# Kernel optimization log

Measured on AMD Instinct MI355X. Metric: run time of the kernel, lower is better.

## Reference

```python
import jax, jax.numpy as jnp
import numpy as np

D = 256
H = 4
HD = D // H


def setup_inputs() -> dict:
    key = jax.random.key(0)
    ks = jax.random.split(key, 12)
    A, T = 64, 512
    s = 1.0 / np.sqrt(D)
    return {
        "features": jax.random.normal(ks[0], (A, T, D), jnp.float32),
        "positions": jax.random.normal(ks[1], (A, T, 2), jnp.float32),
        "Wq": jax.random.normal(ks[2], (D, D), jnp.float32) * s,
        "bq": jnp.zeros((D,), jnp.float32),
        "Wk": jax.random.normal(ks[3], (D, D), jnp.float32) * s,
        "bk": jnp.zeros((D,), jnp.float32),
        "Wv": jax.random.normal(ks[4], (D, D), jnp.float32) * s,
        "bv": jnp.zeros((D,), jnp.float32),
        "Wo": jax.random.normal(ks[5], (D, D), jnp.float32) * s,
        "bo": jnp.zeros((D,), jnp.float32),
        "max_distance": 2,
        "time_window": 64,
    }


def _sparse_mask(positions, max_distance, time_window):
    # positions: [A, T, 2] -> allowed [A, T, T]
    A, T, _ = positions.shape
    diff = positions[:, :, None, :] - positions[:, None, :, :]  # [A,T,T,2]
    dist2 = jnp.sum(diff * diff, axis=-1)                       # [A,T,T]
    t = jnp.arange(T)
    tmask = jnp.abs(t[:, None] - t[None, :]) <= time_window      # [T,T]
    return (dist2 <= float(max_distance) ** 2) & tmask[None]     # [A,T,T]


def reference(features, positions, Wq, bq, Wk, bk, Wv, bv, Wo, bo,
              max_distance, time_window):
    A, T, Dm = features.shape
    allowed = _sparse_mask(positions, max_distance, time_window)  # [A,T,T]
    q = features @ Wq.T + bq
    k = features @ Wk.T + bk
    v = features @ Wv.T + bv
    # split heads: [A, T, H, HD]
    q = q.reshape(A, T, H, HD)
    k = k.reshape(A, T, H, HD)
    v = v.reshape(A, T, H, HD)
    scale = 1.0 / np.sqrt(HD)
    scores = jnp.einsum("athd,ashd->ahts", q, k) * scale          # [A,H,T,T]
    scores = jnp.where(allowed[:, None], scores, -jnp.inf)
    attn = jax.nn.softmax(scores, axis=-1)
    out = jnp.einsum("ahts,ashd->athd", attn, v).reshape(A, T, Dm)
    return out @ Wo.T + bo
```

## Files before the change

### kernel.cpp

```cpp
#include <hip/hip_runtime.h>
#include <hip/hip_bf16.h>
#include <cstdint>
#include <cstddef>

typedef __attribute__((ext_vector_type(8))) _Float16 half8;
typedef __attribute__((ext_vector_type(4))) _Float16 half4v;
typedef __attribute__((ext_vector_type(4))) float floatx4;

#define MFMA16(a, b, c) __builtin_amdgcn_mfma_f32_16x16x32_f16((a), (b), (c), 0, 0, 0)

#define NFEAT 8388608
#define NW    65536

__global__ __launch_bounds__(256) void convert_kernel(
    const float* __restrict__ feat, const float* __restrict__ wq,
    const float* __restrict__ wk, const float* __restrict__ wv,
    const float* __restrict__ wo, _Float16* __restrict__ out)
{
    long tid  = (long)blockIdx.x * blockDim.x + threadIdx.x;
    long base = tid * 4;
    if (base >= (long)NFEAT + 4L * NW) return;
    const float* src;
    long off;
    if (base < NFEAT) { src = feat; off = base; }
    else {
        long r = base - NFEAT;
        int  w = (int)(r >> 16);
        off = r & (NW - 1);
        src = (w == 0) ? wq : (w == 1) ? wk : (w == 2) ? wv : wo;
    }
    float4 v = *(const float4*)(src + off);
    half4v h = { (_Float16)v.x, (_Float16)v.y, (_Float16)v.z, (_Float16)v.w };
    *(half4v*)(out + base) = h;
}

template <bool OUT_HALF>
__device__ __forceinline__ void gemm_core(
    const _Float16* __restrict__ X, const _Float16* __restrict__ W,
    const float* __restrict__ bias, void* __restrict__ Cptr)
{
    __shared__ _Float16 Xs[128 * 40];
    __shared__ _Float16 Wsm[64 * 40];

    const int tid  = threadIdx.x;
    const int lane = tid & 63, wid = tid >> 6;
    const int quad = lane >> 4, l16 = lane & 15;
    const int wm = wid & 1, wn = wid >> 1;
    const int bm = blockIdx.x, bn = blockIdx.y;

    floatx4 acc[4][2] = {};

    const _Float16* Xg = X + (size_t)bm * 128 * 256;
    const _Float16* Wg = W + (size_t)bn * 64 * 256;

    for (int k0 = 0; k0 < 256; k0 += 32) {
#pragma unroll
        for (int i = 0; i < 2; ++i) {
            int c = tid + 256 * i;
            int row = c >> 2, col = (c & 3) * 8;
            *(half8*)(&Xs[row * 40 + col]) =
                *(const half8*)(Xg + (size_t)row * 256 + k0 + col);
        }
        {
            int row = tid >> 2, col = (tid & 3) * 8;
            *(half8*)(&Wsm[row * 40 + col]) =
                *(const half8*)(Wg + (size_t)row * 256 + k0 + col);
        }
        __syncthreads();

        half8 af[4], bf[2];
#pragma unroll
        for (int mi = 0; mi < 4; ++mi)
            af[mi] = *(const half8*)(&Xs[(wm * 64 + mi * 16 + l16) * 40 + quad * 8]);
#pragma unroll
        for (int ni = 0; ni < 2; ++ni)
            bf[ni] = *(const half8*)(&Wsm[(wn * 32 + ni * 16 + l16) * 40 + quad * 8]);
#pragma unroll
        for (int mi = 0; mi < 4; ++mi)
#pragma unroll
            for (int ni = 0; ni < 2; ++ni)
                acc[mi][ni] = MFMA16(af[mi], bf[ni], acc[mi][ni]);
        __syncthreads();
    }

#pragma unroll
    for (int ni = 0; ni < 2; ++ni) {
        int col = bn * 64 + wn * 32 + ni * 16 + l16;
        float bv = bias[col];
#pragma unroll
        for (int mi = 0; mi < 4; ++mi) {
#pragma unroll
            for (int r = 0; r < 4; ++r) {
                int row = bm * 128 + wm * 64 + mi * 16 + quad * 4 + r;
                float v = acc[mi][ni][r] + bv;
                if (OUT_HALF)
                    ((_Float16*)Cptr)[(size_t)row * 256 + col] = (_Float16)v;
                else
                    ((float*)Cptr)[(size_t)row * 256 + col] = v;
            }
        }
    }
}

__global__ __launch_bounds__(256) void qkv_gemm(
    const _Float16* __restrict__ featH, const _Float16* __restrict__ WH,
    const float* __restrict__ bq, const float* __restrict__ bk,
    const float* __restrict__ bv,
    _Float16* __restrict__ Qb, _Float16* __restrict__ Kb, _Float16* __restrict__ Vb)
{
    int z = blockIdx.z;
    const _Float16* W = WH + (size_t)z * NW;
    const float* bias = (z == 0) ? bq : (z == 1) ? bk : bv;
    _Float16* out    = (z == 0) ? Qb : (z == 1) ? Kb : Vb;
    gemm_core<true>(featH, W, bias, out);
}

__global__ __launch_bounds__(256) void out_gemm(
    const _Float16* __restrict__ attnH, const _Float16* __restrict__ WoH,
    const float* __restrict__ bo, float* __restrict__ out)
{
    gemm_core<false>(attnH, WoH, bo, out);
}

__global__ __launch_bounds__(256) void attn_kernel(
    const _Float16* __restrict__ Qb, const _Float16* __restrict__ Kb,
    const _Float16* __restrict__ Vb, const float* __restrict__ positions,
    const int* __restrict__ mdp, const int* __restrict__ twp,
    _Float16* __restrict__ attnb)
{
    const int qt = blockIdx.x, h = blockIdx.y, a = blockIdx.z;
    const int q0 = qt * 64;
    const int s_base = q0 - 64;
    const int tid = threadIdx.x, lane = tid & 63, wid = tid >> 6;
    const int quad = lane >> 4, l16 = lane & 15;

    __shared__ _Float16 KPs[192 * 72];
    __shared__ _Float16 Vt[64 * 200];
    __shared__ float qpos_s[128];
    __shared__ float kpos_s[384];

    const size_t abase = (size_t)a * 512;

#pragma unroll
    for (int i = 0; i < 6; ++i) {
        int c  = tid + 256 * i;
        int si = c >> 3, col = (c & 7) * 8;
        int sr = s_base + si;
        int sc = min(max(sr, 0), 511);
        *(half8*)(&KPs[si * 72 + col]) =
            *(const half8*)(Kb + (abase + sc) * 256 + h * 64 + col);
    }
#pragma unroll
    for (int i = 0; i < 6; ++i) {
        int c  = tid + 256 * i;
        int si = c >> 3, d0 = (c & 7) * 8;
        int sc = min(max(s_base + si, 0), 511);
        half8 v = *(const half8*)(Vb + (abase + sc) * 256 + h * 64 + d0);
#pragma unroll
        for (int j = 0; j < 8; ++j) Vt[(d0 + j) * 200 + si] = v[j];
    }
    if (tid < 128)
        qpos_s[tid] = positions[(abase + q0 + (tid >> 1)) * 2 + (tid & 1)];
    for (int i = tid; i < 384; i += 256) {
        int si = i >> 1;
        int sc = min(max(s_base + si, 0), 511);
        kpos_s[i] = positions[(abase + sc) * 2 + (i & 1)];
    }
    __syncthreads();

    const int md = *mdp, tw = *twp;
    const float md2 = (float)(md * md);

    const size_t qrow = abase + q0 + wid * 16 + l16;
    half8 aq0 = *(const half8*)(Qb + qrow * 256 + h * 64 + quad * 8);
    half8 aq1 = *(const half8*)(Qb + qrow * 256 + h * 64 + 32 + quad * 8);

    float qpx[4], qpy[4];
    int trow[4];
#pragma unroll
    for (int r = 0; r < 4; ++r) {
        int m = wid * 16 + quad * 4 + r;
        trow[r] = q0 + m;
        qpx[r] = qpos_s[m * 2];
        qpy[r] = qpos_s[m * 2 + 1];
    }

    floatx4 S[12];
#pragma unroll
    for (int j = 0; j < 12; ++j) {
        half8 bk0 = *(const half8*)(&KPs[(j * 16 + l16) * 72 + quad * 8]);
        half8 bk1 = *(const half8*)(&KPs[(j * 16 + l16) * 72 + 32 + quad * 8]);
        floatx4 acc = {};
        acc = MFMA16(aq0, bk0, acc);
        acc = MFMA16(aq1, bk1, acc);
        int si = j * 16 + l16;
        int sr = s_base + si;
        float kx = kpos_s[si * 2], ky = kpos_s[si * 2 + 1];
        bool svalid = (sr >= 0) && (sr < 512);
#pragma unroll
        for (int r = 0; r < 4; ++r) {
            float dx = qpx[r] - kx, dy = qpy[r] - ky;
            float d2 = dx * dx + dy * dy;
            int dt = trow[r] - sr; dt = dt < 0 ? -dt : dt;
            bool ok = svalid && (d2 <= md2) && (dt <= tw);
            S[j][r] = ok ? acc[r] * 0.125f : -1e30f;
        }
    }

    float minv[4];
#pragma unroll
    for (int r = 0; r < 4; ++r) {
        float m = -1e30f;
#pragma unroll
        for (int j = 0; j < 12; ++j) m = fmaxf(m, S[j][r]);
        m = fmaxf(m, __shfl_xor(m, 1));
        m = fmaxf(m, __shfl_xor(m, 2));
        m = fmaxf(m, __shfl_xor(m, 4));
        m = fmaxf(m, __shfl_xor(m, 8));
        float l = 0.f;
#pragma unroll
        for (int j = 0; j < 12; ++j) {
            float p = __expf(S[j][r] - m);
            S[j][r] = p;
            l += p;
        }
        l += __shfl_xor(l, 1);
        l += __shfl_xor(l, 2);
        l += __shfl_xor(l, 4);
        l += __shfl_xor(l, 8);
        minv[r] = 1.0f / l;
    }

    __syncthreads();

    _Float16* Ps = KPs + wid * 16 * 200;
#pragma unroll
    for (int j = 0; j < 12; ++j)
#pragma unroll
        for (int r = 0; r < 4; ++r)
            Ps[(quad * 4 + r) * 200 + j * 16 + l16] = (_Float16)(S[j][r] * minv[r]);

    half8 af[6];
#pragma unroll
    for (int k = 0; k < 6; ++k)
        af[k] = *(const half8*)(&Ps[l16 * 200 + k * 32 + quad * 8]);
#pragma unroll
    for (int n = 0; n < 4; ++n) {
        floatx4 accO = {};
#pragma unroll
        for (int k = 0; k < 6; ++k) {
            half8 bv = *(const half8*)(&Vt[(n * 16 + l16) * 200 + k * 32 + quad * 8]);
            accO = MFMA16(af[k], bv, accO);
        }
#pragma unroll
        for (int r = 0; r < 4; ++r) {
            int row = q0 + wid * 16 + quad * 4 + r;
            attnb[(abase + row) * 256 + h * 64 + n * 16 + l16] = (_Float16)accO[r];
        }
    }
}

extern "C" void kernel_launch(void* const* d_in, const int* in_sizes, int n_in,
                              void* d_out, int out_size, void* d_ws, size_t ws_size,
                              hipStream_t stream)
{
    const float* feat = (const float*)d_in[0];
    const float* pos  = (const float*)d_in[1];
    const float* Wq   = (const float*)d_in[2];
    const float* bq   = (const float*)d_in[3];
    const float* Wk   = (const float*)d_in[4];
    const float* bk   = (const float*)d_in[5];
    const float* Wv   = (const float*)d_in[6];
    const float* bv   = (const float*)d_in[7];
    const float* Wo   = (const float*)d_in[8];
    const float* bo   = (const float*)d_in[9];
    const int*   md   = (const int*)d_in[10];
    const int*   tw   = (const int*)d_in[11];
    float*       out  = (float*)d_out;

    _Float16* ws    = (_Float16*)d_ws;
    _Float16* featH = ws;
    _Float16* WH    = featH + NFEAT;
    _Float16* Qb    = WH + 4 * NW;
    _Float16* Kb    = Qb + NFEAT;
    _Float16* Vb    = Kb + NFEAT;
    _Float16* attnH = featH;

    convert_kernel<<<8448, 256, 0, stream>>>(feat, Wq, Wk, Wv, Wo, ws);

    dim3 gqkv(256, 4, 3);
    qkv_gemm<<<gqkv, 256, 0, stream>>>(featH, WH, bq, bk, bv, Qb, Kb, Vb);

    dim3 gattn(8, 4, 64);
    attn_kernel<<<gattn, 256, 0, stream>>>(Qb, Kb, Vb, pos, md, tw, attnH);

    dim3 gout(256, 4, 1);
    out_gemm<<<gout, 256, 0, stream>>>(attnH, WH + 3 * (size_t)NW, bo, out);
}
```

Baseline: 190.8 us.

## Widen GEMM tiles to full N, reorder grid, and streamline attention loads

The projection GEMMs now compute a 128x256 output tile per block (full N) instead of 128x64, so each feature tile is loaded once rather than four times. The grid order is changed so the Q/K/V blocks for the same row-block run adjacently. In attention, the V transpose-load mapping is reordered to improve LDS write patterns, and the position staging in shared memory is replaced by direct global float2 loads. The larger accumulator (32 floatx4 per thread) raises register pressure, and the out GEMM drops to 256 blocks, which may reduce occupancy.

```diff
diff --git a/kernel.cpp b/kernel.cpp
--- a/kernel.cpp
+++ b/kernel.cpp
@@ -35,23 +35,20 @@
 }
 
 template <bool OUT_HALF>
-__device__ __forceinline__ void gemm_core(
+__device__ __forceinline__ void gemm_core2(
     const _Float16* __restrict__ X, const _Float16* __restrict__ W,
-    const float* __restrict__ bias, void* __restrict__ Cptr)
+    const float* __restrict__ bias, void* __restrict__ Cptr, int bm)
 {
     __shared__ _Float16 Xs[128 * 40];
-    __shared__ _Float16 Wsm[64 * 40];
+    __shared__ _Float16 Ws[256 * 40];
 
     const int tid  = threadIdx.x;
     const int lane = tid & 63, wid = tid >> 6;
     const int quad = lane >> 4, l16 = lane & 15;
     const int wm = wid & 1, wn = wid >> 1;
-    const int bm = blockIdx.x, bn = blockIdx.y;
-
-    floatx4 acc[4][2] = {};
-
+
+    floatx4 acc[4][8] = {};
     const _Float16* Xg = X + (size_t)bm * 128 * 256;
-    const _Float16* Wg = W + (size_t)bn * 64 * 256;
 
     for (int k0 = 0; k0 < 256; k0 += 32) {
 #pragma unroll
@@ -61,31 +58,33 @@
             *(half8*)(&Xs[row * 40 + col]) =
                 *(const half8*)(Xg + (size_t)row * 256 + k0 + col);
         }
-        {
-            int row = tid >> 2, col = (tid & 3) * 8;
-            *(half8*)(&Wsm[row * 40 + col]) =
-                *(const half8*)(Wg + (size_t)row * 256 + k0 + col);
+#pragma unroll
+        for (int i = 0; i < 4; ++i) {
+            int c = tid + 256 * i;
+            int row = c >> 2, col = (c & 3) * 8;
+            *(half8*)(&Ws[row * 40 + col]) =
+                *(const half8*)(W + (size_t)row * 256 + k0 + col);
         }
         __syncthreads();
 
-        half8 af[4], bf[2];
+        half8 af[4], bf[8];
 #pragma unroll
         for (int mi = 0; mi < 4; ++mi)
             af[mi] = *(const half8*)(&Xs[(wm * 64 + mi * 16 + l16) * 40 + quad * 8]);
 #pragma unroll
-        for (int ni = 0; ni < 2; ++ni)
-            bf[ni] = *(const half8*)(&Wsm[(wn * 32 + ni * 16 + l16) * 40 + quad * 8]);
+        for (int ni = 0; ni < 8; ++ni)
+            bf[ni] = *(const half8*)(&Ws[(wn * 128 + ni * 16 + l16) * 40 + quad * 8]);
 #pragma unroll
         for (int mi = 0; mi < 4; ++mi)
 #pragma unroll
-            for (int ni = 0; ni < 2; ++ni)
+            for (int ni = 0; ni < 8; ++ni)
                 acc[mi][ni] = MFMA16(af[mi], bf[ni], acc[mi][ni]);
         __syncthreads();
     }
 
 #pragma unroll
-    for (int ni = 0; ni < 2; ++ni) {
-        int col = bn * 64 + wn * 32 + ni * 16 + l16;
+    for (int ni = 0; ni < 8; ++ni) {
+        int col = wn * 128 + ni * 16 + l16;
         float bv = bias[col];
 #pragma unroll
         for (int mi = 0; mi < 4; ++mi) {
@@ -102,24 +101,24 @@
     }
 }
 
-__global__ __launch_bounds__(256) void qkv_gemm(
+__global__ __launch_bounds__(256, 2) void qkv_gemm(
     const _Float16* __restrict__ featH, const _Float16* __restrict__ WH,
     const float* __restrict__ bq, const float* __restrict__ bk,
     const float* __restrict__ bv,
     _Float16* __restrict__ Qb, _Float16* __restrict__ Kb, _Float16* __restrict__ Vb)
 {
-    int z = blockIdx.z;
+    int z = blockIdx.x;
     const _Float16* W = WH + (size_t)z * NW;
     const float* bias = (z == 0) ? bq : (z == 1) ? bk : bv;
     _Float16* out    = (z == 0) ? Qb : (z == 1) ? Kb : Vb;
-    gemm_core<true>(featH, W, bias, out);
-}
-
-__global__ __launch_bounds__(256) void out_gemm(
+    gemm_core2<true>(featH, W, bias, out, blockIdx.y);
+}
+
+__global__ __launch_bounds__(256, 2) void out_gemm(
     const _Float16* __restrict__ attnH, const _Float16* __restrict__ WoH,
     const float* __restrict__ bo, float* __restrict__ out)
 {
-    gemm_core<false>(attnH, WoH, bo, out);
+    gemm_core2<false>(attnH, WoH, bo, out, blockIdx.y);
 }
 
 __global__ __launch_bounds__(256) void attn_kernel(
@@ -136,8 +135,6 @@
 
     __shared__ _Float16 KPs[192 * 72];
     __shared__ _Float16 Vt[64 * 200];
-    __shared__ float qpos_s[128];
-    __shared__ float kpos_s[384];
 
     const size_t abase = (size_t)a * 512;
 
@@ -145,26 +142,19 @@
     for (int i = 0; i < 6; ++i) {
         int c  = tid + 256 * i;
         int si = c >> 3, col = (c & 7) * 8;
-        int sr = s_base + si;
-        int sc = min(max(sr, 0), 511);
+        int sc = min(max(s_base + si, 0), 511);
         *(half8*)(&KPs[si * 72 + col]) =
             *(const half8*)(Kb + (abase + sc) * 256 + h * 64 + col);
     }
 #pragma unroll
     for (int i = 0; i < 6; ++i) {
         int c  = tid + 256 * i;
-        int si = c >> 3, d0 = (c & 7) * 8;
+        int si = c % 192;
+        int d0 = (c / 192) * 8;
         int sc = min(max(s_base + si, 0), 511);
         half8 v = *(const half8*)(Vb + (abase + sc) * 256 + h * 64 + d0);
 #pragma unroll
         for (int j = 0; j < 8; ++j) Vt[(d0 + j) * 200 + si] = v[j];
-    }
-    if (tid < 128)
-        qpos_s[tid] = positions[(abase + q0 + (tid >> 1)) * 2 + (tid & 1)];
-    for (int i = tid; i < 384; i += 256) {
-        int si = i >> 1;
-        int sc = min(max(s_base + si, 0), 511);
-        kpos_s[i] = positions[(abase + sc) * 2 + (i & 1)];
     }
     __syncthreads();
 
@@ -181,8 +171,9 @@
     for (int r = 0; r < 4; ++r) {
         int m = wid * 16 + quad * 4 + r;
         trow[r] = q0 + m;
-        qpx[r] = qpos_s[m * 2];
-        qpy[r] = qpos_s[m * 2 + 1];
+        float2 qp = *(const float2*)(positions + (abase + q0 + m) * 2);
+        qpx[r] = qp.x;
+        qpy[r] = qp.y;
     }
 
     floatx4 S[12];
@@ -195,11 +186,12 @@
         acc = MFMA16(aq1, bk1, acc);
         int si = j * 16 + l16;
         int sr = s_base + si;
-        float kx = kpos_s[si * 2], ky = kpos_s[si * 2 + 1];
+        int sc = min(max(sr, 0), 511);
+        float2 kp = *(const float2*)(positions + (abase + sc) * 2);
         bool svalid = (sr >= 0) && (sr < 512);
 #pragma unroll
         for (int r = 0; r < 4; ++r) {
-            float dx = qpx[r] - kx, dy = qpy[r] - ky;
+            float dx = qpx[r] - kp.x, dy = qpy[r] - kp.y;
             float d2 = dx * dx + dy * dy;
             int dt = trow[r] - sr; dt = dt < 0 ? -dt : dt;
             bool ok = svalid && (d2 <= md2) && (dt <= tw);
@@ -288,12 +280,12 @@
 
     convert_kernel<<<8448, 256, 0, stream>>>(feat, Wq, Wk, Wv, Wo, ws);
 
-    dim3 gqkv(256, 4, 3);
+    dim3 gqkv(3, 256);
     qkv_gemm<<<gqkv, 256, 0, stream>>>(featH, WH, bq, bk, bv, Qb, Kb, Vb);
 
     dim3 gattn(8, 4, 64);
     attn_kernel<<<gattn, 256, 0, stream>>>(Qb, Kb, Vb, pos, md, tw, attnH);
 
-    dim3 gout(256, 4, 1);
+    dim3 gout(1, 256);
     out_gemm<<<gout, 256, 0, stream>>>(attnH, WH + 3 * (size_t)NW, bo, out);
 }
```

New measurement: 187.5 us. No clear change (-1.7%).
